# Kernel optimization log

Measured on AMD Instinct MI355X. Metric: run time of the kernel, lower is better.

## Reference

```python
import jax, jax.numpy as jnp
import numpy as np

N = 100000       # number of atoms/nodes
MUL_IN = 128     # input multiplicity
MUL_OUT = 128    # output multiplicity
LMAX = 3
IR_DIM = (LMAX + 1) ** 2  # 16 spherical channels


def setup_inputs() -> dict:
    key = jax.random.key(0)
    ks = jax.random.split(key, 5)
    x = jax.random.normal(ks[0], (N, MUL_IN, IR_DIM), dtype=jnp.float32)
    w0 = jax.random.normal(ks[1], (MUL_IN, MUL_OUT), dtype=jnp.float32)
    w1 = jax.random.normal(ks[2], (MUL_IN, MUL_OUT), dtype=jnp.float32)
    w2 = jax.random.normal(ks[3], (MUL_IN, MUL_OUT), dtype=jnp.float32)
    w3 = jax.random.normal(ks[4], (MUL_IN, MUL_OUT), dtype=jnp.float32)
    return {"x": x, "w0": w0, "w1": w1, "w2": w2, "w3": w3}


def reference(x, w0, w1, w2, w3):
    # Equivalent to building the block-strided dense weight and doing one matmul:
    # for channel c in degree l: out[n, o, c] = sum_i w_l[i, o] * x[n, i, c]
    weights = [w0, w1, w2, w3]
    # Stack per-channel weights: [IR_DIM, mul_in, mul_out] (w_l repeated 2l+1 times)
    Wc = jnp.concatenate(
        [jnp.broadcast_to(w[None], (2 * l + 1,) + w.shape) for l, w in enumerate(weights)],
        axis=0,
    )
    # x: [N, mul_in, C]; Wc: [C, mul_in, mul_out] -> out: [N, mul_out, C]
    out = jnp.einsum("nic,cio->noc", x, Wc)
    return out
```

## Files before the change

### kernel.cpp

```cpp
#include <hip/hip_runtime.h>
#include <stdint.h>

typedef short short8 __attribute__((ext_vector_type(8)));
typedef float f32x4 __attribute__((ext_vector_type(4)));

#define NPB     100
#define NBLOCKS 1000

__device__ __forceinline__ uint32_t f32_to_bf16_rne(float f) {
    uint32_t u = __builtin_bit_cast(uint32_t, f);
    uint32_t r = u + 0x7FFFu + ((u >> 16) & 1u);
    return r >> 16;
}
__device__ __forceinline__ uint32_t cvt_pk_bf16(float lo, float hi) {
    uint32_t r;
    asm("v_cvt_pk_bf16_f32 %0, %1, %2" : "=v"(r) : "v"(lo), "v"(hi));
    return r;
}

#define GLOAD_LDS16(g, l)                                                  \
    __builtin_amdgcn_global_load_lds(                                      \
        (const __attribute__((address_space(1))) void*)(g),                \
        (__attribute__((address_space(3))) void*)(l), 16, 0, 0)

__global__ void conv_weights(const float* __restrict__ w0, const float* __restrict__ w1,
                             const float* __restrict__ w2, const float* __restrict__ w3,
                             uint16_t* __restrict__ wt) {
    int idx = blockIdx.x * 256 + threadIdx.x;
    int l = idx >> 14;
    int o = (idx >> 7) & 127;
    int i = idx & 127;
    const float* w = (l == 0) ? w0 : (l == 1) ? w1 : (l == 2) ? w2 : w3;
    wt[idx] = (uint16_t)f32_to_bf16_rne(w[i * 128 + o]);
}

__global__ void __launch_bounds__(512, 1)
isl_kernel(const float* __restrict__ x,
           const uint16_t* __restrict__ wt,
           float* __restrict__ out) {
    __shared__ uint8_t ldsbuf[4][8192];
    const int tid  = threadIdx.x;
    const int lane = tid & 63;
    const int wid  = tid >> 6;
    const int r16  = lane & 15;
    const int kg   = lane >> 4;
    const int kx1  = kg & 1;

    short8 wfr[4][4];
    {
        const uint16_t* wb = wt + (size_t)(wid * 16 + r16) * 128 + kg * 8;
        #pragma unroll
        for (int l = 0; l < 4; ++l)
            #pragma unroll
            for (int ks = 0; ks < 4; ++ks)
                wfr[l][ks] = *(const short8*)(wb + l * 16384 + ks * 32);
    }

    const int n0 = blockIdx.x * NPB;
    const int srcg = tid ^ (((tid >> 5) & 1) << 2);
    const uint8_t* xg = (const uint8_t*)(x + (size_t)n0 * 2048) + (size_t)srcg * 16;

    #pragma unroll
    for (int r = 0; r < 3; ++r)
        GLOAD_LDS16(xg + (size_t)r * 8192, &ldsbuf[r][wid * 1024]);
    asm volatile("s_waitcnt vmcnt(0)" ::: "memory");
    __builtin_amdgcn_s_barrier();

    float* po_base = out + (size_t)n0 * 2048 + (size_t)(wid * 16 + kg * 4) * 16 + r16;

    #pragma unroll 1
    for (int r = 0; r < NPB; ++r) {
        if (r > 0) {
            if (r <= NPB - 3)
                asm volatile("s_waitcnt vmcnt(14)" ::: "memory");
            else
                asm volatile("s_waitcnt vmcnt(2)" ::: "memory");
            __builtin_amdgcn_s_barrier();
        }
        if (r + 3 < NPB)
            GLOAD_LDS16(xg + (size_t)(r + 3) * 8192, &ldsbuf[(r + 3) & 3][wid * 1024]);

        const float* rowp = (const float*)&ldsbuf[r & 3][0];
        short8 xb[4];
        #pragma unroll
        for (int ks = 0; ks < 4; ++ks) {
            float f[8];
            #pragma unroll
            for (int j = 0; j < 8; ++j)
                f[j] = rowp[((ks * 32 + kg * 8 + j) ^ kx1) * 16 + r16];
            uint32_t q[4];
            #pragma unroll
            for (int h = 0; h < 4; ++h)
                q[h] = cvt_pk_bf16(f[2 * h], f[2 * h + 1]);
            xb[ks] = *(const short8*)q;
        }
        f32x4 acc[4] = {{0,0,0,0},{0,0,0,0},{0,0,0,0},{0,0,0,0}};
        #pragma unroll
        for (int l = 0; l < 4; ++l)
            #pragma unroll
            for (int ks = 0; ks < 4; ++ks)
                acc[l] = __builtin_amdgcn_mfma_f32_16x16x32_bf16(wfr[l][ks], xb[ks], acc[l], 0, 0, 0);

        float* po = po_base + (size_t)r * 2048;
        #pragma unroll
        for (int rr = 0; rr < 4; ++rr) {
            float v = acc[0][rr];
            v = (r16 >= 1) ? acc[1][rr] : v;
            v = (r16 >= 4) ? acc[2][rr] : v;
            v = (r16 >= 9) ? acc[3][rr] : v;
            po[rr * 16] = v;
        }
    }
}

extern "C" void kernel_launch(void* const* d_in, const int* in_sizes, int n_in,
                              void* d_out, int out_size, void* d_ws, size_t ws_size,
                              hipStream_t stream) {
    const float* x  = (const float*)d_in[0];
    const float* w0 = (const float*)d_in[1];
    const float* w1 = (const float*)d_in[2];
    const float* w2 = (const float*)d_in[3];
    const float* w3 = (const float*)d_in[4];
    uint16_t* wt = (uint16_t*)d_ws;
    float* out = (float*)d_out;

    conv_weights<<<256, 256, 0, stream>>>(w0, w1, w2, w3, wt);
    isl_kernel<<<NBLOCKS, 512, 0, stream>>>(x, wt, out);
}
```

Before: 342.8 us.

## Process two nodes per iteration with each wave covering two output tiles

Each wave now computes 32 output channels (two 16-wide MFMA tiles) for one of two nodes handled per iteration, instead of 16 channels for a single node. Each converted x fragment read from LDS feeds twice as many MFMAs, and the loop runs half as many barrier/wait steps, with two prefetch loads per step and a doubled LDS ring. The cost is twice as many weight fragments held in registers, and the vmcnt thresholds had to be retuned for the larger number of in-flight loads and stores.

```diff
diff --git a/kernel.cpp b/kernel.cpp
--- a/kernel.cpp
+++ b/kernel.cpp
@@ -5,6 +5,7 @@
 typedef float f32x4 __attribute__((ext_vector_type(4)));
 
 #define NPB     100
+#define NPH     50
 #define NBLOCKS 1000
 
 __device__ __forceinline__ uint32_t f32_to_bf16_rne(float f) {
@@ -38,22 +39,25 @@
 isl_kernel(const float* __restrict__ x,
            const uint16_t* __restrict__ wt,
            float* __restrict__ out) {
-    __shared__ uint8_t ldsbuf[4][8192];
-    const int tid  = threadIdx.x;
-    const int lane = tid & 63;
-    const int wid  = tid >> 6;
-    const int r16  = lane & 15;
-    const int kg   = lane >> 4;
-    const int kx1  = kg & 1;
+    __shared__ uint8_t ldsbuf[4][16384];
+    const int tid   = threadIdx.x;
+    const int lane  = tid & 63;
+    const int wid   = tid >> 6;
+    const int rhalf = wid >> 2;
+    const int og    = (wid & 3) * 32;
+    const int r16   = lane & 15;
+    const int kg    = lane >> 4;
+    const int kx1   = kg & 1;
 
-    short8 wfr[4][4];
-    {
-        const uint16_t* wb = wt + (size_t)(wid * 16 + r16) * 128 + kg * 8;
+    short8 wfr[2][4][4];
+    #pragma unroll
+    for (int t = 0; t < 2; ++t) {
+        const uint16_t* wb = wt + (size_t)(og + t * 16 + r16) * 128 + kg * 8;
         #pragma unroll
         for (int l = 0; l < 4; ++l)
             #pragma unroll
             for (int ks = 0; ks < 4; ++ks)
-                wfr[l][ks] = *(const short8*)(wb + l * 16384 + ks * 32);
+                wfr[t][l][ks] = *(const short8*)(wb + l * 16384 + ks * 32);
     }
 
     const int n0 = blockIdx.x * NPB;
@@ -61,26 +65,34 @@
     const uint8_t* xg = (const uint8_t*)(x + (size_t)n0 * 2048) + (size_t)srcg * 16;
 
     #pragma unroll
-    for (int r = 0; r < 3; ++r)
-        GLOAD_LDS16(xg + (size_t)r * 8192, &ldsbuf[r][wid * 1024]);
+    for (int p = 0; p < 3; ++p)
+        #pragma unroll
+        for (int h = 0; h < 2; ++h)
+            GLOAD_LDS16(xg + (size_t)(2 * p + h) * 8192,
+                        &ldsbuf[p][h * 8192 + wid * 1024]);
     asm volatile("s_waitcnt vmcnt(0)" ::: "memory");
     __builtin_amdgcn_s_barrier();
 
-    float* po_base = out + (size_t)n0 * 2048 + (size_t)(wid * 16 + kg * 4) * 16 + r16;
+    float* po_base = out + (size_t)(n0 + rhalf) * 2048 +
+                     (size_t)(og + kg * 4) * 16 + r16;
 
     #pragma unroll 1
-    for (int r = 0; r < NPB; ++r) {
-        if (r > 0) {
-            if (r <= NPB - 3)
-                asm volatile("s_waitcnt vmcnt(14)" ::: "memory");
+    for (int p = 0; p < NPH; ++p) {
+        if (p > 0) {
+            if (p <= NPH - 3)
+                asm volatile("s_waitcnt vmcnt(28)" ::: "memory");
             else
-                asm volatile("s_waitcnt vmcnt(2)" ::: "memory");
+                asm volatile("s_waitcnt vmcnt(24)" ::: "memory");
             __builtin_amdgcn_s_barrier();
         }
-        if (r + 3 < NPB)
-            GLOAD_LDS16(xg + (size_t)(r + 3) * 8192, &ldsbuf[(r + 3) & 3][wid * 1024]);
+        if (p + 3 < NPH) {
+            GLOAD_LDS16(xg + (size_t)(2 * (p + 3)) * 8192,
+                        &ldsbuf[(p + 3) & 3][wid * 1024]);
+            GLOAD_LDS16(xg + (size_t)(2 * (p + 3) + 1) * 8192,
+                        &ldsbuf[(p + 3) & 3][8192 + wid * 1024]);
+        }
 
-        const float* rowp = (const float*)&ldsbuf[r & 3][0];
+        const float* rowp = (const float*)&ldsbuf[p & 3][rhalf * 8192];
         short8 xb[4];
         #pragma unroll
         for (int ks = 0; ks < 4; ++ks) {
@@ -94,21 +106,33 @@
                 q[h] = cvt_pk_bf16(f[2 * h], f[2 * h + 1]);
             xb[ks] = *(const short8*)q;
         }
-        f32x4 acc[4] = {{0,0,0,0},{0,0,0,0},{0,0,0,0},{0,0,0,0}};
+
+        f32x4 acc[2][4];
         #pragma unroll
-        for (int l = 0; l < 4; ++l)
+        for (int t = 0; t < 2; ++t)
             #pragma unroll
-            for (int ks = 0; ks < 4; ++ks)
-                acc[l] = __builtin_amdgcn_mfma_f32_16x16x32_bf16(wfr[l][ks], xb[ks], acc[l], 0, 0, 0);
+            for (int l = 0; l < 4; ++l)
+                acc[t][l] = (f32x4){0.f, 0.f, 0.f, 0.f};
+        #pragma unroll
+        for (int t = 0; t < 2; ++t)
+            #pragma unroll
+            for (int l = 0; l < 4; ++l)
+                #pragma unroll
+                for (int ks = 0; ks < 4; ++ks)
+                    acc[t][l] = __builtin_amdgcn_mfma_f32_16x16x32_bf16(
+                        wfr[t][l][ks], xb[ks], acc[t][l], 0, 0, 0);
 
-        float* po = po_base + (size_t)r * 2048;
+        float* po = po_base + (size_t)(2 * p) * 2048;
         #pragma unroll
-        for (int rr = 0; rr < 4; ++rr) {
-            float v = acc[0][rr];
-            v = (r16 >= 1) ? acc[1][rr] : v;
-            v = (r16 >= 4) ? acc[2][rr] : v;
-            v = (r16 >= 9) ? acc[3][rr] : v;
-            po[rr * 16] = v;
+        for (int t = 0; t < 2; ++t) {
+            #pragma unroll
+            for (int rr = 0; rr < 4; ++rr) {
+                float v = acc[t][0][rr];
+                v = (r16 >= 1) ? acc[t][1][rr] : v;
+                v = (r16 >= 4) ? acc[t][2][rr] : v;
+                v = (r16 >= 9) ? acc[t][3][rr] : v;
+                po[(t * 16 + rr) * 16] = v;
+            }
         }
     }
 }
```

Result: no change. 344.7 us (+0.5%).
